# Kernel tuning notes

Measured on AMD Instinct MI355X. Metric: run time of the kernel, lower is better.

## Reference

```python
import jax, jax.numpy as jnp
import numpy as np

D = 20          # embedding dim (hardcoded in original module)
N_REL = 200     # relation vocab size (table has N_REL+1 rows)
N_TIME = 365    # time embedding table size
L = 3           # propagation layers
E = 2_000_000   # edges per layer
N = 1_000_000   # node-slot pool per layer
B = 64          # batch size
N_ENT = 1_000_003


def setup_inputs() -> dict:
    key = jax.random.key(0)
    ks = jax.random.split(key, 16)
    src_idx = jax.random.randint(ks[0], (L, E), 0, N, dtype=jnp.int32)
    dst_idx = jax.random.randint(ks[1], (L, E), 0, N, dtype=jnp.int32)
    rel_idx = jax.random.randint(ks[2], (L, E), 0, N_REL + 1, dtype=jnp.int32)
    qrel_idx = jax.random.randint(ks[3], (L, E), 0, N_REL + 1, dtype=jnp.int32)
    # signed relative time (edge_time - query_time); abs() must stay < N_TIME
    rel_time = jax.random.randint(ks[4], (L, E), -(N_TIME - 1), N_TIME, dtype=jnp.int32)
    node_batch = jax.random.randint(ks[5], (N,), 0, B, dtype=jnp.int32)
    node_ent = jnp.arange(N, dtype=jnp.int32)  # unique entity per final node slot
    s = 0.1
    rela_embed = jax.random.normal(ks[6], (N_REL + 1, D), jnp.float32) * s
    time_embed = jax.random.normal(ks[7], (N_TIME, D), jnp.float32) * s
    w_att1 = jax.random.normal(ks[8], (30, 3 * D), jnp.float32) * s
    w_att2 = jax.random.normal(ks[9], (1, 30), jnp.float32) * s
    w_past = jax.random.normal(ks[10], (D, D), jnp.float32) * s
    w_now = jax.random.normal(ks[11], (D, D), jnp.float32) * s
    w_future = jax.random.normal(ks[12], (D, D), jnp.float32) * s
    w_cls = jax.random.normal(ks[13], (D,), jnp.float32) * s
    b_cls = jnp.zeros((), jnp.float32)
    return dict(src_idx=src_idx, dst_idx=dst_idx, rel_idx=rel_idx,
                qrel_idx=qrel_idx, rel_time=rel_time, node_batch=node_batch,
                node_ent=node_ent, rela_embed=rela_embed, time_embed=time_embed,
                w_att1=w_att1, w_att2=w_att2, w_past=w_past, w_now=w_now,
                w_future=w_future, w_cls=w_cls, b_cls=b_cls,
                batch_size=B, n_ent=N_ENT)


def reference(src_idx, dst_idx, rel_idx, qrel_idx, rel_time, node_batch,
              node_ent, rela_embed, time_embed, w_att1, w_att2, w_past,
              w_now, w_future, w_cls, b_cls, batch_size, n_ent):
    n_layers = src_idx.shape[0]
    n_nodes = node_batch.shape[0]
    d = rela_embed.shape[1]
    hidden = jnp.zeros((n_nodes, d), dtype=rela_embed.dtype)
    for l in range(n_layers):
        rt = rel_time[l]                         # [E] signed relative time
        h_src = hidden[src_idx[l]]               # [E, D] gather
        r_emb = rela_embed[rel_idx[l]]           # [E, D]
        t_emb = time_embed[jnp.abs(rt)]          # [E, D]
        embed_rel = h_src + r_emb + t_emb
        # conditional time-branch MLP (mask-partitioned linear, same math as
        # the original's boolean-masked assignments)
        fut = embed_rel @ w_future.T
        now = embed_rel @ w_now.T
        pst = embed_rel @ w_past.T
        transformed = jnp.where((rt > 0)[:, None], fut,
                       jnp.where((rt == 0)[:, None], now, pst))
        # attention over concat(hidden_src, rel_emb, query_rel_emb)  [E, 3D]
        att_in = jnp.concatenate([h_src, r_emb, rela_embed[qrel_idx[l]]], axis=1)
        score = jax.nn.sigmoid(jax.nn.relu(att_in @ w_att1.T) @ w_att2.T)  # [E,1]
        msg = score * transformed                # [E, D]
        hidden = jax.ops.segment_sum(msg, dst_idx[l], num_segments=n_nodes)
        hidden = jax.nn.leaky_relu(hidden)       # default slope 0.01, as torch
    result = hidden @ w_cls + b_cls              # [N]
    score_all = jnp.zeros((batch_size, n_ent), dtype=result.dtype)
    score_all = score_all.at[node_batch, node_ent].set(result)
    return score_all
```

## Files before the change

kernel.cpp:

```cpp
#include <hip/hip_runtime.h>
#include <hip/hip_bf16.h>
#include <hip/hip_fp16.h>
#include <cstdint>

#define DD 20
#define HID 30
#define NB_SCAN 1024
#define HROW 32

typedef unsigned int  u32;
typedef unsigned short u16;
typedef _Float16 hf2 __attribute__((ext_vector_type(2)));

__device__ __forceinline__ hf2 as_hf2(u32 u){ union{u32 u; hf2 v;} c; c.u=u; return c.v; }
__device__ __forceinline__ u32 pkhf(float a, float b){
  union{hf2 v; u32 u;} c; c.v[0]=(_Float16)a; c.v[1]=(_Float16)b; return c.u;
}
__device__ __forceinline__ float lo16f(u32 u){ union{u16 s; _Float16 h;} c; c.s=(u16)(u&0xFFFF); return (float)c.h; }
__device__ __forceinline__ float hi16f(u32 u){ union{u16 s; _Float16 h;} c; c.s=(u16)(u>>16); return (float)c.h; }

__device__ __forceinline__ float dot10p(const u32* hh, const u32* __restrict__ w, float acc){
#if __has_builtin(__builtin_amdgcn_fdot2)
#pragma unroll
  for (int c=0;c<10;c++) acc = __builtin_amdgcn_fdot2(as_hf2(hh[c]), as_hf2(w[c]), acc, false);
#else
#pragma unroll
  for (int c=0;c<10;c++) acc += lo16f(hh[c])*lo16f(w[c]) + hi16f(hh[c])*hi16f(w[c]);
#endif
  return acc;
}

__device__ __forceinline__ void load20(const float* __restrict__ p, float* r){
  const float4* q = (const float4*)p;
#pragma unroll
  for (int i=0;i<5;i++){ float4 v=q[i]; r[4*i+0]=v.x; r[4*i+1]=v.y; r[4*i+2]=v.z; r[4*i+3]=v.w; }
}

__device__ __forceinline__ u32 pkbf(float a, float b){
  u32 ua=__float_as_uint(a); ua=(ua+0x7FFFu+((ua>>16)&1u))>>16;
  u32 ub=__float_as_uint(b); ub=(ub+0x7FFFu+((ub>>16)&1u))>>16;
  return ua | (ub<<16);
}

__global__ void k_prep(const float* __restrict__ rela, const float* __restrict__ w1,
                       const float* __restrict__ wp, const float* __restrict__ wn,
                       const float* __restrict__ wf,
                       float* __restrict__ W3, float* __restrict__ AR, float* __restrict__ AQ,
                       int nrel){
  int t = blockIdx.x*blockDim.x + threadIdx.x;
  if (t < 3*DD*DD){
    int s = t/(DD*DD), idx = t%(DD*DD);
    W3[t] = (s==0)?wp[idx]:((s==1)?wn[idx]:wf[idx]);
  }
  if (t < nrel*HID){
    int r=t/HID, j=t-r*HID;
    float sr=0.f, sq=0.f;
#pragma unroll
    for (int k=0;k<DD;k++){
      float e = rela[r*DD+k];
      sr += e*w1[j*3*DD + DD + k];
      sq += e*w1[j*3*DD + 2*DD + k];
    }
    AR[r*32+j]=sr; AQ[r*32+j]=sq;
  }
}

__global__ void k_rwtw(const float* __restrict__ rela, const float* __restrict__ timee,
                       const float* __restrict__ W3,
                       float* __restrict__ RW, float* __restrict__ TW,
                       int nrel, int ntime){
  int t = blockIdx.x*blockDim.x+threadIdx.x;
  int totR = 3*nrel*DD, totT = 3*ntime*DD;
  if (t < totR){
    int sel = t/(nrel*DD); int rem = t - sel*nrel*DD; int r = rem/DD; int i = rem - r*DD;
    const float* w = W3 + sel*DD*DD + i*DD;
    const float* e = rela + (size_t)r*DD;
    float s=0.f;
#pragma unroll
    for (int k=0;k<DD;k++) s += e[k]*w[k];
    RW[t]=s;
  }
  if (t < totT){
    int sel = t/(ntime*DD); int rem = t - sel*ntime*DD; int tt = rem/DD; int i = rem - tt*DD;
    const float* w = W3 + sel*DD*DD + i*DD;
    const float* e = timee + (size_t)tt*DD;
    float s=0.f;
#pragma unroll
    for (int k=0;k<DD;k++) s += e[k]*w[k];
    TW[t]=s;
  }
}

__global__ void k_rt(const float* __restrict__ rela, const float* __restrict__ timee,
                     const float* __restrict__ W3, float* __restrict__ RT,
                     int nrel, int ntime){
  int row = blockIdx.x*blockDim.x+threadIdx.x;
  int tot = 3*nrel*ntime;
  if (row>=tot) return;
  int per = nrel*ntime;
  int sel = row/per; int rem = row - sel*per; int r = rem/ntime; int t = rem - r*ntime;
  float e[DD], tv[DD];
  load20(rela + (size_t)r*DD, e);
  load20(timee + (size_t)t*DD, tv);
#pragma unroll
  for (int k=0;k<DD;k++) e[k]+=tv[k];
  const float* W = W3 + sel*DD*DD;
  float o[DD];
#pragma unroll
  for (int i=0;i<DD;i++){
    const float4* wr = (const float4*)(W + i*DD);
    float s=0.f;
#pragma unroll
    for (int c=0;c<5;c++){ float4 w=wr[c]; s += e[4*c]*w.x + e[4*c+1]*w.y + e[4*c+2]*w.z + e[4*c+3]*w.w; }
    o[i]=s;
  }
  float4* op=(float4*)(RT + (size_t)row*DD);
#pragma unroll
  for (int c=0;c<5;c++){ float4 v; v.x=o[4*c]; v.y=o[4*c+1]; v.z=o[4*c+2]; v.w=o[4*c+3]; op[c]=v; }
}

__global__ void __launch_bounds__(256) k_pre(const int* __restrict__ dst, int* __restrict__ cnt,
        int* __restrict__ rank, int E, int N,
        float4* __restrict__ dout4, size_t nd4,
        float4* __restrict__ bF, size_t nf4){
  int g=blockIdx.x, tid=threadIdx.x;
  int half=gridDim.x>>1;
  if (g & 1){
    int stride=half*256;
    int E2=2*E;
    for (int e=(g>>1)*256+tid; e<E2; e+=stride){
      int l=(e>=E)?1:0;
      rank[e]=atomicAdd(&cnt[(size_t)l*N+dst[e]],1);
    }
  } else {
    float4 z=make_float4(0.f,0.f,0.f,0.f);
    size_t i=(size_t)(g>>1)*256+tid, st=(size_t)half*256;
    for (size_t k=i;k<nd4;k+=st) dout4[k]=z;
    for (size_t k=i;k<nf4;k+=st) bF[k]=z;
  }
}

__global__ void k_scan_part(const int* __restrict__ cnt, int* __restrict__ part, int M, int C){
  __shared__ int sm[256];
  int b=blockIdx.x, t=threadIdx.x;
  int lo=b*C, hi=lo+C; if (hi>M) hi=M; if (lo>M) lo=M;
  int s=0;
  for (int i=lo+t; i<hi; i+=256) s+=cnt[i];
  sm[t]=s; __syncthreads();
  for (int o=128;o>0;o>>=1){ if (t<o) sm[t]+=sm[t+o]; __syncthreads(); }
  if (t==0) part[b]=sm[0];
}

__global__ void k_scan_top(int* __restrict__ part, int* __restrict__ listc){
  __shared__ int sm[NB_SCAN];
  int t=threadIdx.x;
  if (t==0) *listc=0;
  int v=part[t]; sm[t]=v; __syncthreads();
  for (int o=1;o<NB_SCAN;o<<=1){
    int u=(t>=o)?sm[t-o]:0; __syncthreads();
    sm[t]+=u; __syncthreads();
  }
  part[t]=sm[t]-v;
}

template<int ZM>
__global__ void k_scan_write(const int* __restrict__ cnt, const int* __restrict__ part,
                             int* __restrict__ rowptr, int M, int C, int base,
                             u16* __restrict__ zb0, u16* __restrict__ zb1, int Nsplit,
                             float* __restrict__ zres){
  __shared__ int sm[256];
  int b=blockIdx.x, t=threadIdx.x;
  int lo=b*C, hi=lo+C; if (hi>M) hi=M; if (lo>M) lo=M;
  int run=part[b]+base;
  for (int bb=lo; bb<hi; bb+=256){
    int i=bb+t;
    int v=(i<hi)?cnt[i]:0;
    if (i<hi && v==0){
      if (ZM==1){
        u16* o=(i<Nsplit)? zb0+(size_t)i*HROW : zb1+(size_t)(i-Nsplit)*HROW;
        uint4 z=make_uint4(0u,0u,0u,0u);
        uint4* o4=(uint4*)o;
        o4[0]=z; o4[1]=z; *((uint2*)(o4+2))=make_uint2(0u,0u);
      } else if (ZM==2){
        zres[i]=0.f;
      }
    }
    sm[t]=v; __syncthreads();
    for (int o=1;o<256;o<<=1){
      int u=(t>=o)?sm[t-o]:0; __syncthreads();
      sm[t]+=u; __syncthreads();
    }
    if (i<hi) rowptr[i]=run+sm[t]-v;
    int tot=sm[255];
    __syncthreads();
    run+=tot;
  }
  if (hi==M && t==0) rowptr[M]=run;
}

__global__ void __launch_bounds__(256) k_scat01(const int* __restrict__ src,const int* __restrict__ dst,
  const int* __restrict__ rel,const int* __restrict__ qrel,const int* __restrict__ rtm,
  const int* __restrict__ rank,const int* __restrict__ rowptr,int4* __restrict__ recs,int E,int N){
  int e=blockIdx.x*blockDim.x+threadIdx.x;
  if (e>=2*E) return;
  int l=(e>=E)?1:0;
  int d=dst[e];
  int pos=rowptr[(size_t)l*N+d]+rank[e];
  recs[pos]=make_int4(src[e], rel[e]|(qrel[e]<<16), rtm[e], d);
}

__global__ void __launch_bounds__(256) k_scat2(const int* __restrict__ src,const int* __restrict__ dst,
  const int* __restrict__ rel,const int* __restrict__ qrel,const int* __restrict__ rtm,
  const int* __restrict__ rank,const int* __restrict__ rowptr2,int4* __restrict__ recs,int E){
  int e=blockIdx.x*blockDim.x+threadIdx.x;
  if (e>=E) return;
  int d=dst[e];
  int pos=rowptr2[d]+rank[e];
  recs[pos]=make_int4(src[e], rel[e]|(qrel[e]<<16), rtm[e], d);
}

template<bool HASH,bool FINAL,bool HIST>
__global__ void __launch_bounds__(256) k_fused(
    const int4* __restrict__ recs,
    const u16* __restrict__ hin, u16* __restrict__ hout, float* __restrict__ bufF,
    const float* __restrict__ RW, const float* __restrict__ TW,
    const float* __restrict__ AR, const float* __restrict__ AQ,
    const float* __restrict__ w1, const float* __restrict__ w2, const float* __restrict__ W3,
    int E, int nrel, int ntime,
    const int* __restrict__ hB_dst, int* __restrict__ hB_cnt, int* __restrict__ hB_rank, int hB_E,
    const float* __restrict__ wcls, float* __restrict__ res,
    int* __restrict__ list, int* __restrict__ listc)
{
  int lb;
  if (HIST){
    int g=blockIdx.x;
    int r3=g%3, b3=g/3;
    if (r3==2){
      int H=gridDim.x/3;
      int stride=H*256;
      for (int e=b3*256+threadIdx.x; e<hB_E; e+=stride)
        hB_rank[e]=atomicAdd(&hB_cnt[hB_dst[e]],1);
      return;
    }
    lb=b3*2+r3;
  } else lb=blockIdx.x;
  int bstart=lb*256;
  if (bstart>=E) return;

  __shared__ u32   sW1hp[HID*10];
  __shared__ u32   sW3p[3*DD*10];
  __shared__ float sW2[32];
  __shared__ u32   smsg[256*10];
  __shared__ int   sdst[256];
  __shared__ int   s_prevdst, s_nextdst;
  if (HASH){
    for (int t=threadIdx.x; t<HID*10; t+=blockDim.x){
      int j=t/10, c=t-j*10;
      sW1hp[t]=pkhf(w1[j*3*DD+2*c], w1[j*3*DD+2*c+1]);
    }
    for (int t=threadIdx.x; t<3*DD*10; t+=blockDim.x){
      int i=t/10, c=t-i*10;
      sW3p[t]=pkhf(W3[i*DD+2*c], W3[i*DD+2*c+1]);
    }
  }
  if (threadIdx.x<HID) sW2[threadIdx.x]=w2[threadIdx.x];

  int tid = threadIdx.x;
  int bsize = E - bstart; if (bsize>256) bsize=256;
  int j = bstart + tid;
  bool active = (tid < bsize);

  if (tid==0){
    s_prevdst = (bstart>0) ? recs[-1 + (ptrdiff_t)bstart].w : -1;
    s_nextdst = (bstart+bsize < E) ? recs[bstart+bsize].w : -1;
  }
  __syncthreads();

  int dstv = -1;
  float m[DD];
  if (active){
    int4 rc = recs[j];
    int s = rc.x;
    int r = rc.y & 0xFFFF;
    int q = ((unsigned)rc.y) >> 16;
    int t = rc.z;
    dstv  = rc.w;
    int sel = (t>0)?2:((t==0)?1:0);
    int ta = (t<0)?-t:t;

    u32 hh[10];
    if (HASH){
      const uint4* hp=(const uint4*)(hin+(size_t)s*HROW);
      uint4 A=hp[0], B=hp[1]; uint2 Cc=*((const uint2*)(hp+2));
      hh[0]=A.x; hh[1]=A.y; hh[2]=A.z; hh[3]=A.w;
      hh[4]=B.x; hh[5]=B.y; hh[6]=B.z; hh[7]=B.w;
      hh[8]=Cc.x; hh[9]=Cc.y;
    }

    float z=0.f;
    {
      const float4* ap=(const float4*)(AR+(size_t)r*32);
      const float4* qp=(const float4*)(AQ+(size_t)q*32);
#pragma unroll
      for (int c=0;c<7;c++){
        float4 x=ap[c], y=qp[c];
        float s4[4]={x.x+y.x, x.y+y.y, x.z+y.z, x.w+y.w};
#pragma unroll
        for (int u=0;u<4;u++){
          int jj=4*c+u;
          float sum=s4[u];
          if (HASH) sum = dot10p(hh, &sW1hp[jj*10], sum);
          z += fmaxf(sum,0.f)*sW2[jj];
        }
      }
      float2 x2=*(const float2*)(AR+(size_t)r*32+28);
      float2 y2=*(const float2*)(AQ+(size_t)q*32+28);
      float s0=x2.x+y2.x, s1=x2.y+y2.y;
      if (HASH){
        s0 = dot10p(hh, &sW1hp[28*10], s0);
        s1 = dot10p(hh, &sW1hp[29*10], s1);
      }
      z += fmaxf(s0,0.f)*sW2[28] + fmaxf(s1,0.f)*sW2[29];
    }
    float score = 1.f/(1.f+__expf(-z));

    const float4* rwp=(const float4*)(RW + ((size_t)(sel*nrel+r))*DD);
    const float4* twp=(const float4*)(TW + ((size_t)(sel*ntime+ta))*DD);
#pragma unroll
    for (int c=0;c<5;c++){
      float4 a4=rwp[c], b4=twp[c];
      float mv[4]={a4.x+b4.x, a4.y+b4.y, a4.z+b4.z, a4.w+b4.w};
      if (HASH){
#pragma unroll
        for (int u=0;u<4;u++)
          mv[u] = dot10p(hh, &sW3p[(sel*DD+4*c+u)*10], mv[u]);
      }
#pragma unroll
      for (int u=0;u<4;u++) m[4*c+u]=score*mv[u];
      smsg[tid*10+2*c]  =pkbf(m[4*c+0],m[4*c+1]);
      smsg[tid*10+2*c+1]=pkbf(m[4*c+2],m[4*c+3]);
    }
  }
  sdst[tid] = active ? dstv : -2;
  __syncthreads();

  if (!active) return;
  bool isHead = (tid==0) ? (s_prevdst != dstv) : (sdst[tid-1] != dstv);
  if (!(isHead || tid==0)) return;
  int k=tid+1;
  for (; k<bsize && sdst[k]==dstv; ++k){
    const u32* row=&smsg[k*10];
#pragma unroll
    for (int i2=0;i2<10;i2++){
      u32 w=row[i2];
      m[2*i2]  +=__uint_as_float(w<<16);
      m[2*i2+1]+=__uint_as_float(w&0xFFFF0000u);
    }
  }
  bool crossStart = (tid==0 && !isHead);
  bool crossEnd   = (k==bsize) && (s_nextdst==dstv);
  if (crossStart || crossEnd){
    float* o = bufF + (size_t)dstv*DD;
#pragma unroll
    for (int i=0;i<DD;i++) atomicAdd(o+i, m[i]);
    if (!FINAL && isHead){
      int p = atomicAdd(listc,1);
      list[p] = dstv;
    }
  } else {
    if (!FINAL){
      u32 o10[10];
#pragma unroll
      for (int i2=0;i2<10;i2++){
        float x0=m[2*i2], x1=m[2*i2+1];
        x0=fmaxf(x0,0.01f*x0); x1=fmaxf(x1,0.01f*x1);
        o10[i2]=pkhf(x0,x1);
      }
      uint4* hp=(uint4*)(hout+(size_t)dstv*HROW);
      hp[0]=make_uint4(o10[0],o10[1],o10[2],o10[3]);
      hp[1]=make_uint4(o10[4],o10[5],o10[6],o10[7]);
      *((uint2*)(hp+2))=make_uint2(o10[8],o10[9]);
    } else {
      float rsum=0.f;
#pragma unroll
      for (int i=0;i<DD;i++){ float x=fmaxf(m[i],0.01f*m[i]); rsum += x*wcls[i]; }
      res[dstv] = rsum;
    }
  }
}

__global__ void __launch_bounds__(256) k_fixup(float* __restrict__ bufF, u16* __restrict__ hout,
   const int* __restrict__ list,const int* __restrict__ listc){
  int c=*listc;
  for (int i=blockIdx.x*blockDim.x+threadIdx.x; i<c; i+=gridDim.x*blockDim.x){
    int n=list[i];
    float* p=bufF+(size_t)n*DD;
    float v[DD];
#pragma unroll
    for (int jj=0;jj<DD;jj++){ v[jj]=p[jj]; p[jj]=0.f; }
    u32 o10[10];
#pragma unroll
    for (int i2=0;i2<10;i2++){
      float x0=v[2*i2], x1=v[2*i2+1];
      x0=fmaxf(x0,0.01f*x0); x1=fmaxf(x1,0.01f*x1);
      o10[i2]=pkhf(x0,x1);
    }
    uint4* hp=(uint4*)(hout+(size_t)n*HROW);
    hp[0]=make_uint4(o10[0],o10[1],o10[2],o10[3]);
    hp[1]=make_uint4(o10[4],o10[5],o10[6],o10[7]);
    *((uint2*)(hp+2))=make_uint2(o10[8],o10[9]);
  }
}

__global__ void __launch_bounds__(256) k_out(const float* __restrict__ res,
   const float* __restrict__ bufF, const float* __restrict__ wcls, const float* __restrict__ bcls,
   const int* __restrict__ nb, const int* __restrict__ ne, const int* __restrict__ nentp,
   float* __restrict__ out, int N){
  int n=blockIdx.x*blockDim.x+threadIdx.x;
  if (n>=N) return;
  float acc = res[n] + bcls[0];
  const float4* q=(const float4*)(bufF+(size_t)n*DD);
#pragma unroll
  for (int c=0;c<5;c++){
    float4 v=q[c];
    acc += fmaxf(v.x,0.01f*v.x)*wcls[4*c]   + fmaxf(v.y,0.01f*v.y)*wcls[4*c+1]
         + fmaxf(v.z,0.01f*v.z)*wcls[4*c+2] + fmaxf(v.w,0.01f*v.w)*wcls[4*c+3];
  }
  long long stride = nentp[0];
  out[(long long)nb[n]*stride + ne[n]] = acc;
}

template<bool HASH>
__global__ void __launch_bounds__(256) k_edge(
    const int* __restrict__ src, const int* __restrict__ dst,
    const int* __restrict__ rel, const int* __restrict__ qrel,
    const int* __restrict__ rtm,
    const float* __restrict__ hin, float* __restrict__ hout,
    const float* __restrict__ RT, const float* __restrict__ AR, const float* __restrict__ AQ,
    const float* __restrict__ w1, const float* __restrict__ w2, const float* __restrict__ W3,
    int E, int nrel, int ntime)
{
  __shared__ float sW1h[HID*DD];
  __shared__ float sW2[32];
  __shared__ float sW3[3*DD*DD];
  for (int t=threadIdx.x; t<HID*DD; t+=blockDim.x){ int j=t/DD,k=t-j*DD; sW1h[t]=w1[j*3*DD+k]; }
  if (threadIdx.x<HID) sW2[threadIdx.x]=w2[threadIdx.x];
  for (int t=threadIdx.x; t<3*DD*DD; t+=blockDim.x) sW3[t]=W3[t];
  __syncthreads();
  int e = blockIdx.x*blockDim.x+threadIdx.x;
  if (e>=E) return;
  int s=src[e], d=dst[e], r=rel[e], q=qrel[e], t=rtm[e];
  int sel = (t>0)?2:((t==0)?1:0);
  int ta = (t<0)?-t:t;
  float h[DD];
  if (HASH){
    load20(hin+(size_t)s*DD, h);
#pragma unroll
    for (int i=0;i<DD;i++) h[i]=fmaxf(h[i],0.01f*h[i]);
  }
  float a[HID];
  {
    const float4* ap=(const float4*)(AR+(size_t)r*32);
    const float4* qp=(const float4*)(AQ+(size_t)q*32);
#pragma unroll
    for (int c=0;c<7;c++){
      float4 x=ap[c], y=qp[c];
      a[4*c+0]=x.x+y.x; a[4*c+1]=x.y+y.y; a[4*c+2]=x.z+y.z; a[4*c+3]=x.w+y.w;
    }
    float2 x=*(const float2*)(AR+(size_t)r*32+28);
    float2 y=*(const float2*)(AQ+(size_t)q*32+28);
    a[28]=x.x+y.x; a[29]=x.y+y.y;
  }
  if (HASH){
#pragma unroll
    for (int j=0;j<HID;j++){
      const float4* wr=(const float4*)&sW1h[j*DD];
      float sum=a[j];
#pragma unroll
      for (int c=0;c<5;c++){ float4 w=wr[c]; sum += h[4*c]*w.x+h[4*c+1]*w.y+h[4*c+2]*w.z+h[4*c+3]*w.w; }
      a[j]=sum;
    }
  }
  float z=0.f;
#pragma unroll
  for (int j=0;j<HID;j++) z += fmaxf(a[j],0.f)*sW2[j];
  float score = 1.f/(1.f+__expf(-z));
  float tr[DD];
  load20(RT + ((size_t)(sel*nrel+r)*ntime + ta)*DD, tr);
  if (HASH){
    const float* Ws = sW3 + sel*DD*DD;
#pragma unroll
    for (int i=0;i<DD;i++){
      const float4* wr=(const float4*)(Ws+i*DD);
      float sum=tr[i];
#pragma unroll
      for (int c=0;c<5;c++){ float4 w=wr[c]; sum += h[4*c]*w.x+h[4*c+1]*w.y+h[4*c+2]*w.z+h[4*c+3]*w.w; }
      tr[i]=sum;
    }
  }
  float* o = hout + (size_t)d*DD;
#pragma unroll
  for (int i=0;i<DD;i++) atomicAdd(o+i, score*tr[i]);
}

__global__ void k_result(const float* __restrict__ h, const float* __restrict__ wcls,
                         const float* __restrict__ bcls, float* __restrict__ res, int N){
  int i = blockIdx.x*blockDim.x+threadIdx.x;
  if (i>=N) return;
  float acc = bcls[0];
  const float4* q=(const float4*)(h+(size_t)i*DD);
#pragma unroll
  for (int c=0;c<5;c++){
    float4 v=q[c];
    float x0=fmaxf(v.x,0.01f*v.x), x1=fmaxf(v.y,0.01f*v.y);
    float x2=fmaxf(v.z,0.01f*v.z), x3=fmaxf(v.w,0.01f*v.w);
    acc += x0*wcls[4*c]+x1*wcls[4*c+1]+x2*wcls[4*c+2]+x3*wcls[4*c+3];
  }
  res[i]=acc;
}

__global__ void k_scatter(const float* __restrict__ res, const int* __restrict__ nb,
                          const int* __restrict__ ne, const int* __restrict__ nentp,
                          float* __restrict__ out, int N){
  int i=blockIdx.x*blockDim.x+threadIdx.x;
  if (i>=N) return;
  long long stride = nentp[0];
  out[(long long)nb[i]*stride + ne[i]] = res[i];
}

extern "C" void kernel_launch(void* const* d_in, const int* in_sizes, int n_in,
                              void* d_out, int out_size, void* d_ws, size_t ws_size,
                              hipStream_t stream){
  const int*   src =(const int*)d_in[0];
  const int*   dst =(const int*)d_in[1];
  const int*   rel =(const int*)d_in[2];
  const int*   qrel=(const int*)d_in[3];
  const int*   rtm =(const int*)d_in[4];
  const int*   nb  =(const int*)d_in[5];
  const int*   ne  =(const int*)d_in[6];
  const float* rela=(const float*)d_in[7];
  const float* timee=(const float*)d_in[8];
  const float* w1  =(const float*)d_in[9];
  const float* w2  =(const float*)d_in[10];
  const float* wp  =(const float*)d_in[11];
  const float* wn  =(const float*)d_in[12];
  const float* wf  =(const float*)d_in[13];
  const float* wcls=(const float*)d_in[14];
  const float* bcls=(const float*)d_in[15];
  const int*   nentp=(const int*)d_in[17];

  const int Lc=3;
  int LE=in_sizes[0]; int E=LE/Lc;
  int N=in_sizes[5];
  int nrel=in_sizes[7]/DD;
  int ntime=in_sizes[8]/DD;

  auto al=[](size_t x){ return (x+(size_t)255)&~(size_t)255; };
  size_t szBufH=al((size_t)N*HROW*2);
  size_t szBuf =al((size_t)N*DD*4);
  size_t szRW  =al((size_t)3*nrel*DD*4);
  size_t szTW  =al((size_t)3*ntime*DD*4);
  size_t szRTf =al((size_t)3*nrel*ntime*DD*4);
  size_t szA   =al((size_t)nrel*32*4);
  size_t szW3  =al((size_t)3*DD*DD*4);
  size_t szRow =al(((size_t)3*N+3)*4);
  size_t szRank=al((size_t)LE*4);
  size_t szCnt =al((size_t)Lc*N*4);
  size_t szRecs=al((size_t)LE*16);
  size_t szPart=al((size_t)NB_SCAN*4);
  size_t szList=al((size_t)(131072+16)*4);
  size_t szRes =al((size_t)N*4);
  size_t need = 2*szBufH+szBuf+szRW+szTW+2*szA+szW3+szRow+szRank+szCnt+szRecs+szPart+szList+szRes;

  dim3 blk(256);
  int prepTot = (3*DD*DD > nrel*HID) ? 3*DD*DD : nrel*HID;
  int rtTot=3*nrel*ntime;
  int rwtwTot = 3*ntime*DD;

  if (ws_size >= need){
    char* base=(char*)d_ws;
    size_t off=0;
    u16*   b0 =(u16*)(base+off);    off+=szBufH;
    u16*   b1 =(u16*)(base+off);    off+=szBufH;
    float* bufF=(float*)(base+off); off+=szBuf;
    float* RW  =(float*)(base+off); off+=szRW;
    float* TW  =(float*)(base+off); off+=szTW;
    float* AR  =(float*)(base+off); off+=szA;
    float* AQ  =(float*)(base+off); off+=szA;
    float* W3  =(float*)(base+off); off+=szW3;
    int*   rowptr=(int*)(base+off); off+=szRow;
    int*   rowptr2=rowptr+(size_t)2*N+1;
    int*   rank=(int*)(base+off);  off+=szRank;
    int*   cnt =(int*)(base+off);  off+=szCnt;
    int4*  recs=(int4*)(base+off); off+=szRecs;
    int*   part=(int*)(base+off);  off+=szPart;
    int*   listc=(int*)(base+off);
    int*   list =listc+16;          off+=szList;
    float* res =(float*)(base+off); off+=szRes;

    float* dout=(float*)d_out;

    (void)hipMemsetAsync(cnt,0,(size_t)Lc*N*4,stream);
    k_prep<<<dim3((prepTot+255)/256),blk,0,stream>>>(rela,w1,wp,wn,wf,W3,AR,AQ,nrel);
    k_rwtw<<<dim3((rwtwTot+255)/256),blk,0,stream>>>(rela,timee,W3,RW,TW,nrel,ntime);

    size_t nd4=(size_t)out_size>>2;
    size_t nb4=(size_t)N*DD/4;
    k_pre<<<dim3(8192),blk,0,stream>>>(dst,cnt,rank,E,N,(float4*)dout,nd4,
                                       (float4*)bufF,nb4);

    int LB=(E+255)/256;
    int H=(LB+1)/2;

    {
      int M=2*N, C=(M+NB_SCAN-1)/NB_SCAN;
      k_scan_part<<<dim3(NB_SCAN),blk,0,stream>>>(cnt,part,M,C);
      k_scan_top<<<dim3(1),dim3(NB_SCAN),0,stream>>>(part,listc);
      k_scan_write<1><<<dim3(NB_SCAN),blk,0,stream>>>(cnt,part,rowptr,M,C,0,b0,b1,N,nullptr);
    }
    k_scat01<<<dim3((2*E+255)/256),blk,0,stream>>>(src,dst,rel,qrel,rtm,rank,rowptr,recs,E,N);

    k_fused<false,false,true><<<dim3(3*H),blk,0,stream>>>(recs,nullptr,b0,bufF,
        RW,TW,AR,AQ,w1,w2,W3,E,nrel,ntime,
        dst+(size_t)2*E,cnt+(size_t)2*N,rank+(size_t)2*E,E,
        wcls,res,list,listc);
    k_fixup<<<dim3(128),blk,0,stream>>>(bufF,b0,list,listc);

    {
      int C=(N+NB_SCAN-1)/NB_SCAN;
      k_scan_part<<<dim3(NB_SCAN),blk,0,stream>>>(cnt+(size_t)2*N,part,N,C);
      k_scan_top<<<dim3(1),dim3(NB_SCAN),0,stream>>>(part,listc);
      k_scan_write<2><<<dim3(NB_SCAN),blk,0,stream>>>(cnt+(size_t)2*N,part,rowptr2,N,C,2*E,
                                                      nullptr,nullptr,0,res);
    }
    k_scat2<<<dim3(LB),blk,0,stream>>>(src+(size_t)2*E,dst+(size_t)2*E,rel+(size_t)2*E,
        qrel+(size_t)2*E,rtm+(size_t)2*E,rank+(size_t)2*E,rowptr2,recs,E);

    k_fused<true,false,false><<<dim3(LB),blk,0,stream>>>(recs+(size_t)E,b0,b1,bufF,
        RW,TW,AR,AQ,w1,w2,W3,E,nrel,ntime,
        nullptr,nullptr,nullptr,0,
        wcls,res,list,listc);
    k_fixup<<<dim3(128),blk,0,stream>>>(bufF,b1,list,listc);

    k_fused<true,true,false><<<dim3(LB),blk,0,stream>>>(recs+(size_t)2*E,b1,nullptr,bufF,
        RW,TW,AR,AQ,w1,w2,W3,E,nrel,ntime,
        nullptr,nullptr,nullptr,0,
        wcls,res,list,listc);

    k_out<<<dim3((N+255)/256),blk,0,stream>>>(res,bufF,wcls,bcls,nb,ne,nentp,dout,N);
  } else {
    char* base=(char*)d_out; float* res=(float*)d_ws;
    size_t off=0;
    float* buf0=(float*)(base+off); off+=szBuf;
    float* buf1=(float*)(base+off); off+=szBuf;
    float* RT  =(float*)(base+off); off+=szRTf;
    float* AR  =(float*)(base+off); off+=szA;
    float* AQ  =(float*)(base+off); off+=szA;
    float* W3  =(float*)(base+off); off+=szW3;
    k_prep<<<dim3((prepTot+255)/256),blk,0,stream>>>(rela,w1,wp,wn,wf,W3,AR,AQ,nrel);
    k_rt<<<dim3((rtTot+255)/256),blk,0,stream>>>(rela,timee,W3,RT,nrel,ntime);
    dim3 egrid((E+255)/256);
    dim3 ngrid((N+255)/256);
    (void)hipMemsetAsync(buf0,0,(size_t)N*DD*4,stream);
    k_edge<false><<<egrid,blk,0,stream>>>(src,dst,rel,qrel,rtm,nullptr,buf0,RT,AR,AQ,w1,w2,W3,E,nrel,ntime);
    (void)hipMemsetAsync(buf1,0,(size_t)N*DD*4,stream);
    k_edge<true><<<egrid,blk,0,stream>>>(src+(size_t)E,dst+(size_t)E,rel+(size_t)E,qrel+(size_t)E,rtm+(size_t)E,
                                         buf0,buf1,RT,AR,AQ,w1,w2,W3,E,nrel,ntime);
    (void)hipMemsetAsync(buf0,0,(size_t)N*DD*4,stream);
    k_edge<true><<<egrid,blk,0,stream>>>(src+(size_t)2*E,dst+(size_t)2*E,rel+(size_t)2*E,qrel+(size_t)2*E,rtm+(size_t)2*E,
                                         buf1,buf0,RT,AR,AQ,w1,w2,W3,E,nrel,ntime);
    k_result<<<ngrid,blk,0,stream>>>(buf0,wcls,bcls,res,N);
    (void)hipMemsetAsync(d_out,0,(size_t)out_size*sizeof(float),stream);
    k_scatter<<<ngrid,blk,0,stream>>>(res,nb,ne,nentp,(float*)d_out,N);
  }
}
```

Before: 970.9 us.

## Write final scores directly from fused kernel and fixup, drop k_out pass

The final layer's fused kernel now applies the classifier and bias and scatters the score straight into the output, and nodes with no in-edges get the bias written during the scan. Boundary nodes are handled by a FINAL variant of the fixup kernel, which uses its own list and counter. This removes the intermediate res buffer and the full N-wide k_out pass that reread res and bufF. In exchange, the fused kernel performs scattered output writes, and each layer's boundary list is capped at 32768 entries per slot.

Measured after the change: 961.0 us, median of 2. No clear change (-1.0%).

```diff
diff --git a/kernel.cpp b/kernel.cpp
--- a/kernel.cpp
+++ b/kernel.cpp
@@ -154,7 +154,7 @@
 __global__ void k_scan_top(int* __restrict__ part, int* __restrict__ listc){
   __shared__ int sm[NB_SCAN];
   int t=threadIdx.x;
-  if (t==0) *listc=0;
+  if (t==0){ listc[0]=0; listc[1]=0; listc[2]=0; listc[3]=0; }
   int v=part[t]; sm[t]=v; __syncthreads();
   for (int o=1;o<NB_SCAN;o<<=1){
     int u=(t>=o)?sm[t-o]:0; __syncthreads();
@@ -167,7 +167,9 @@
 __global__ void k_scan_write(const int* __restrict__ cnt, const int* __restrict__ part,
                              int* __restrict__ rowptr, int M, int C, int base,
                              u16* __restrict__ zb0, u16* __restrict__ zb1, int Nsplit,
-                             float* __restrict__ zres){
+                             const int* __restrict__ nb, const int* __restrict__ ne,
+                             const int* __restrict__ nentp, const float* __restrict__ bcls,
+                             float* __restrict__ dout){
   __shared__ int sm[256];
   int b=blockIdx.x, t=threadIdx.x;
   int lo=b*C, hi=lo+C; if (hi>M) hi=M; if (lo>M) lo=M;
@@ -182,7 +184,8 @@
         uint4* o4=(uint4*)o;
         o4[0]=z; o4[1]=z; *((uint2*)(o4+2))=make_uint2(0u,0u);
       } else if (ZM==2){
-        zres[i]=0.f;
+        long long stride=nentp[0];
+        dout[(long long)nb[i]*stride + ne[i]] = bcls[0];
       }
     }
     sm[t]=v; __syncthreads();
@@ -228,7 +231,9 @@
     const float* __restrict__ w1, const float* __restrict__ w2, const float* __restrict__ W3,
     int E, int nrel, int ntime,
     const int* __restrict__ hB_dst, int* __restrict__ hB_cnt, int* __restrict__ hB_rank, int hB_E,
-    const float* __restrict__ wcls, float* __restrict__ res,
+    const float* __restrict__ wcls, const float* __restrict__ bcls,
+    const int* __restrict__ nbv, const int* __restrict__ nev, const int* __restrict__ nentp,
+    float* __restrict__ outp,
     int* __restrict__ list, int* __restrict__ listc)
 {
   int lb;
@@ -363,7 +368,7 @@
     float* o = bufF + (size_t)dstv*DD;
 #pragma unroll
     for (int i=0;i<DD;i++) atomicAdd(o+i, m[i]);
-    if (!FINAL && isHead){
+    if (isHead){
       int p = atomicAdd(listc,1);
       list[p] = dstv;
     }
@@ -381,53 +386,48 @@
       hp[1]=make_uint4(o10[4],o10[5],o10[6],o10[7]);
       *((uint2*)(hp+2))=make_uint2(o10[8],o10[9]);
     } else {
-      float rsum=0.f;
+      float rsum=bcls[0];
 #pragma unroll
       for (int i=0;i<DD;i++){ float x=fmaxf(m[i],0.01f*m[i]); rsum += x*wcls[i]; }
-      res[dstv] = rsum;
-    }
-  }
-}
-
+      long long stride = nentp[0];
+      outp[(long long)nbv[dstv]*stride + nev[dstv]] = rsum;
+    }
+  }
+}
+
+template<bool FINAL>
 __global__ void __launch_bounds__(256) k_fixup(float* __restrict__ bufF, u16* __restrict__ hout,
-   const int* __restrict__ list,const int* __restrict__ listc){
+   const float* __restrict__ wcls, const float* __restrict__ bcls,
+   const int* __restrict__ nb, const int* __restrict__ ne, const int* __restrict__ nentp,
+   float* __restrict__ out,
+   const int* __restrict__ list, const int* __restrict__ listc){
   int c=*listc;
   for (int i=blockIdx.x*blockDim.x+threadIdx.x; i<c; i+=gridDim.x*blockDim.x){
     int n=list[i];
     float* p=bufF+(size_t)n*DD;
-    float v[DD];
-#pragma unroll
-    for (int jj=0;jj<DD;jj++){ v[jj]=p[jj]; p[jj]=0.f; }
-    u32 o10[10];
-#pragma unroll
-    for (int i2=0;i2<10;i2++){
-      float x0=v[2*i2], x1=v[2*i2+1];
-      x0=fmaxf(x0,0.01f*x0); x1=fmaxf(x1,0.01f*x1);
-      o10[i2]=pkhf(x0,x1);
-    }
-    uint4* hp=(uint4*)(hout+(size_t)n*HROW);
-    hp[0]=make_uint4(o10[0],o10[1],o10[2],o10[3]);
-    hp[1]=make_uint4(o10[4],o10[5],o10[6],o10[7]);
-    *((uint2*)(hp+2))=make_uint2(o10[8],o10[9]);
-  }
-}
-
-__global__ void __launch_bounds__(256) k_out(const float* __restrict__ res,
-   const float* __restrict__ bufF, const float* __restrict__ wcls, const float* __restrict__ bcls,
-   const int* __restrict__ nb, const int* __restrict__ ne, const int* __restrict__ nentp,
-   float* __restrict__ out, int N){
-  int n=blockIdx.x*blockDim.x+threadIdx.x;
-  if (n>=N) return;
-  float acc = res[n] + bcls[0];
-  const float4* q=(const float4*)(bufF+(size_t)n*DD);
-#pragma unroll
-  for (int c=0;c<5;c++){
-    float4 v=q[c];
-    acc += fmaxf(v.x,0.01f*v.x)*wcls[4*c]   + fmaxf(v.y,0.01f*v.y)*wcls[4*c+1]
-         + fmaxf(v.z,0.01f*v.z)*wcls[4*c+2] + fmaxf(v.w,0.01f*v.w)*wcls[4*c+3];
-  }
-  long long stride = nentp[0];
-  out[(long long)nb[n]*stride + ne[n]] = acc;
+    if (FINAL){
+      float rsum=bcls[0];
+#pragma unroll
+      for (int jj=0;jj<DD;jj++){ float v=p[jj]; float x=fmaxf(v,0.01f*v); rsum+=x*wcls[jj]; }
+      long long stride=nentp[0];
+      out[(long long)nb[n]*stride+ne[n]]=rsum;
+    } else {
+      float v[DD];
+#pragma unroll
+      for (int jj=0;jj<DD;jj++){ v[jj]=p[jj]; p[jj]=0.f; }
+      u32 o10[10];
+#pragma unroll
+      for (int i2=0;i2<10;i2++){
+        float x0=v[2*i2], x1=v[2*i2+1];
+        x0=fmaxf(x0,0.01f*x0); x1=fmaxf(x1,0.01f*x1);
+        o10[i2]=pkhf(x0,x1);
+      }
+      uint4* hp=(uint4*)(hout+(size_t)n*HROW);
+      hp[0]=make_uint4(o10[0],o10[1],o10[2],o10[3]);
+      hp[1]=make_uint4(o10[4],o10[5],o10[6],o10[7]);
+      *((uint2*)(hp+2))=make_uint2(o10[8],o10[9]);
+    }
+  }
 }
 
 template<bool HASH>
@@ -569,8 +569,7 @@
   size_t szRecs=al((size_t)LE*16);
   size_t szPart=al((size_t)NB_SCAN*4);
   size_t szList=al((size_t)(131072+16)*4);
-  size_t szRes =al((size_t)N*4);
-  size_t need = 2*szBufH+szBuf+szRW+szTW+2*szA+szW3+szRow+szRank+szCnt+szRecs+szPart+szList+szRes;
+  size_t need = 2*szBufH+szBuf+szRW+szTW+2*szA+szW3+szRow+szRank+szCnt+szRecs+szPart+szList;
 
   dim3 blk(256);
   int prepTot = (3*DD*DD > nrel*HID) ? 3*DD*DD : nrel*HID;
@@ -596,7 +595,6 @@
     int*   part=(int*)(base+off);  off+=szPart;
     int*   listc=(int*)(base+off);
     int*   list =listc+16;          off+=szList;
-    float* res =(float*)(base+off); off+=szRes;
 
     float* dout=(float*)d_out;
 
@@ -616,22 +614,24 @@
       int M=2*N, C=(M+NB_SCAN-1)/NB_SCAN;
       k_scan_part<<<dim3(NB_SCAN),blk,0,stream>>>(cnt,part,M,C);
       k_scan_top<<<dim3(1),dim3(NB_SCAN),0,stream>>>(part,listc);
-      k_scan_write<1><<<dim3(NB_SCAN),blk,0,stream>>>(cnt,part,rowptr,M,C,0,b0,b1,N,nullptr);
+      k_scan_write<1><<<dim3(NB_SCAN),blk,0,stream>>>(cnt,part,rowptr,M,C,0,
+          b0,b1,N, nullptr,nullptr,nullptr,nullptr,nullptr);
     }
     k_scat01<<<dim3((2*E+255)/256),blk,0,stream>>>(src,dst,rel,qrel,rtm,rank,rowptr,recs,E,N);
 
     k_fused<false,false,true><<<dim3(3*H),blk,0,stream>>>(recs,nullptr,b0,bufF,
         RW,TW,AR,AQ,w1,w2,W3,E,nrel,ntime,
         dst+(size_t)2*E,cnt+(size_t)2*N,rank+(size_t)2*E,E,
-        wcls,res,list,listc);
-    k_fixup<<<dim3(128),blk,0,stream>>>(bufF,b0,list,listc);
+        wcls,bcls,nb,ne,nentp,dout,
+        list,listc);
+    k_fixup<false><<<dim3(128),blk,0,stream>>>(bufF,b0,wcls,bcls,nb,ne,nentp,dout,list,listc);
 
     {
       int C=(N+NB_SCAN-1)/NB_SCAN;
       k_scan_part<<<dim3(NB_SCAN),blk,0,stream>>>(cnt+(size_t)2*N,part,N,C);
       k_scan_top<<<dim3(1),dim3(NB_SCAN),0,stream>>>(part,listc);
       k_scan_write<2><<<dim3(NB_SCAN),blk,0,stream>>>(cnt+(size_t)2*N,part,rowptr2,N,C,2*E,
-                                                      nullptr,nullptr,0,res);
+          nullptr,nullptr,0, nb,ne,nentp,bcls,dout);
     }
     k_scat2<<<dim3(LB),blk,0,stream>>>(src+(size_t)2*E,dst+(size_t)2*E,rel+(size_t)2*E,
         qrel+(size_t)2*E,rtm+(size_t)2*E,rank+(size_t)2*E,rowptr2,recs,E);
@@ -639,15 +639,16 @@
     k_fused<true,false,false><<<dim3(LB),blk,0,stream>>>(recs+(size_t)E,b0,b1,bufF,
         RW,TW,AR,AQ,w1,w2,W3,E,nrel,ntime,
         nullptr,nullptr,nullptr,0,
-        wcls,res,list,listc);
-    k_fixup<<<dim3(128),blk,0,stream>>>(bufF,b1,list,listc);
+        wcls,bcls,nb,ne,nentp,dout,
+        list+32768,listc+1);
+    k_fixup<false><<<dim3(128),blk,0,stream>>>(bufF,b1,wcls,bcls,nb,ne,nentp,dout,list+32768,listc+1);
 
     k_fused<true,true,false><<<dim3(LB),blk,0,stream>>>(recs+(size_t)2*E,b1,nullptr,bufF,
         RW,TW,AR,AQ,w1,w2,W3,E,nrel,ntime,
         nullptr,nullptr,nullptr,0,
-        wcls,res,list,listc);
-
-    k_out<<<dim3((N+255)/256),blk,0,stream>>>(res,bufF,wcls,bcls,nb,ne,nentp,dout,N);
+        wcls,bcls,nb,ne,nentp,dout,
+        list+65536,listc+2);
+    k_fixup<true><<<dim3(128),blk,0,stream>>>(bufF,nullptr,wcls,bcls,nb,ne,nentp,dout,list+65536,listc+2);
   } else {
     char* base=(char*)d_out; float* res=(float*)d_ws;
     size_t off=0;
```
